# Kernel tuning notes

Measured on AMD Instinct MI355X. Metric: run time of the kernel, lower is better.

Reference implementation:

```python
import jax, jax.numpy as jnp
import numpy as np

LOG_STD_MAX = 2.0
LOG_STD_MIN = -5.0
N_EXPERTS = 16
TOPK = 4
OBS = 512
ACT = 256
BATCH = 16384


def setup_inputs() -> dict:
    key = jax.random.key(0)
    ks = jax.random.split(key, 7)
    s_obs = 1.0 / np.sqrt(OBS)
    return {
        "x": jax.random.normal(ks[0], (BATCH, OBS), dtype=jnp.float32),
        "router_w": jax.random.uniform(ks[1], (N_EXPERTS, OBS), jnp.float32, -s_obs, s_obs),
        "router_b": jax.random.uniform(ks[2], (N_EXPERTS,), jnp.float32, -s_obs, s_obs),
        "mean_w": jax.random.uniform(ks[3], (N_EXPERTS, ACT, OBS), jnp.float32, -s_obs, s_obs),
        "mean_b": jax.random.uniform(ks[4], (N_EXPERTS, ACT), jnp.float32, -s_obs, s_obs),
        "log_std_w": jax.random.uniform(ks[5], (N_EXPERTS, ACT, OBS), jnp.float32, -s_obs, s_obs),
        "log_std_b": jax.random.uniform(ks[6], (N_EXPERTS, ACT), jnp.float32, -s_obs, s_obs),
        "router_noise": 0,
    }


def reference(x, router_w, router_b, mean_w, mean_b, log_std_w, log_std_b, router_noise):
    # router_noise=0 -> deterministic path (training-time noise omitted)
    B = x.shape[0]
    router_logits = x @ router_w.T + router_b                    # [B, E]
    router_probs = jax.nn.softmax(router_logits, axis=-1)         # [B, E]
    topk_probs, topk_idx = jax.lax.top_k(router_probs, TOPK)      # [B, K]
    sparse_probs = jnp.zeros_like(router_probs).at[
        jnp.arange(B)[:, None], topk_idx
    ].set(topk_probs)                                             # [B, E]

    # all-expert dense stack: [B, E, A]
    expert_out = jnp.einsum("bo,eao->bea", x, mean_w) + mean_b
    log_std_out = jnp.einsum("bo,eao->bea", x, log_std_w) + log_std_b

    w = sparse_probs[:, :, None]                                  # [B, E, 1]
    mean = jnp.sum(expert_out * w, axis=1)                        # [B, A]
    log_std = jnp.sum(log_std_out * w, axis=1)                    # [B, A]
    log_std = jnp.tanh(log_std)
    log_std = LOG_STD_MIN + 0.5 * (LOG_STD_MAX - LOG_STD_MIN) * (log_std + 1.0)
    return mean, log_std
```

## Files before the change

### kernel.cpp

```cpp
#include <hip/hip_runtime.h>
#include <math.h>

#define BB   16384
#define OBS  512
#define NE   16
#define ACTD 256
#define TK   4

#define WS_ROWLIST_OFF  ((size_t)64)
#define WS_PROBLIST_OFF (WS_ROWLIST_OFF + (size_t)NE * BB * 4)
#define WS_SLOT_OFF     (WS_PROBLIST_OFF + (size_t)NE * BB * 4)
#define WS_XBF_OFF      (WS_SLOT_OFF + (size_t)NE * BB * 4)
#define WS_WM_OFF       (WS_XBF_OFF + (size_t)BB * OBS * 2)
#define WS_WL_OFF       (WS_WM_OFF + (size_t)NE * ACTD * OBS * 2)
#define WS_PART_OFF     (WS_WL_OFF + (size_t)NE * ACTD * OBS * 2)
#define WS_NEEDED_A2    (WS_PART_OFF + (size_t)2 * BB * TK * ACTD * 2)

typedef __attribute__((ext_vector_type(8))) short short8;
typedef __attribute__((ext_vector_type(4))) float floatx4;

__device__ __forceinline__ ushort f2bf(float f) {
    union { float f; unsigned u; } v; v.f = f;
    unsigned r = v.u + 0x7fffu + ((v.u >> 16) & 1u);
    return (ushort)(r >> 16);
}
__device__ __forceinline__ float bf2f(ushort u) {
    union { unsigned u; float f; } v; v.u = ((unsigned)u) << 16;
    return v.f;
}
__device__ __forceinline__ float lstd_act(float v) {
    return -5.f + 7.f * __builtin_amdgcn_rcpf(1.f + __expf(-2.f * v));
}

__global__ __launch_bounds__(256) void cvt2_bf16(
    const float* __restrict__ s0, const float* __restrict__ s1,
    ushort* __restrict__ d0, ushort* __restrict__ d1, int n4,
    int* __restrict__ counts)
{
    if (blockIdx.x == 0 && threadIdx.x < NE) counts[threadIdx.x] = 0;
    const int i = blockIdx.x * 256 + threadIdx.x;
    const float4* src = (i < n4) ? ((const float4*)s0 + i) : ((const float4*)s1 + (i - n4));
    ushort4* dst = (i < n4) ? ((ushort4*)d0 + i) : ((ushort4*)d1 + (i - n4));
    float4 v = *src;
    ushort4 o;
    o.x = f2bf(v.x); o.y = f2bf(v.y); o.z = f2bf(v.z); o.w = f2bf(v.w);
    *dst = o;
}

__global__ __launch_bounds__(256) void router_kernel(
    const float* __restrict__ x, const float* __restrict__ rw,
    const float* __restrict__ rb,
    int* __restrict__ counts, int* __restrict__ rowlist,
    float* __restrict__ problist, int* __restrict__ slot_of,
    ushort* __restrict__ xbf, int do_aux)
{
    __shared__ float wlds[NE * OBS];
    __shared__ int   lcnt[NE], lbase[NE];
    __shared__ int   s_e[64], s_lpos[64];
    __shared__ float s_p[64];

    const float4* rw4 = (const float4*)rw;
    float4* wl4 = (float4*)wlds;
    #pragma unroll
    for (int i = 0; i < 8; ++i) wl4[threadIdx.x + 256 * i] = rw4[threadIdx.x + 256 * i];
    if (threadIdx.x < NE) lcnt[threadIdx.x] = 0;
    __syncthreads();

    const int wave = threadIdx.x >> 6;
    const int lane = threadIdx.x & 63;
    const int q    = lane >> 4;
    const int i16  = lane & 15;
    const int row  = blockIdx.x * 16 + wave * 4 + q;

    const float4* xr = (const float4*)(x + (size_t)row * OBS);
    float4 xv[8];
    #pragma unroll
    for (int s = 0; s < 8; ++s) xv[s] = xr[s * 16 + i16];

    if (do_aux) {
        ushort4* xo = (ushort4*)(xbf + (size_t)row * OBS);
        #pragma unroll
        for (int s = 0; s < 8; ++s) {
            ushort4 o;
            o.x = f2bf(xv[s].x); o.y = f2bf(xv[s].y);
            o.z = f2bf(xv[s].z); o.w = f2bf(xv[s].w);
            xo[s * 16 + i16] = o;
        }
    }

    float p[NE];
    float m = -1e30f;
    #pragma unroll
    for (int e = 0; e < NE; ++e) {
        const float4* wep = (const float4*)(wlds + e * OBS);
        float d = 0.f;
        #pragma unroll
        for (int s = 0; s < 8; ++s) {
            float4 wv = wep[s * 16 + i16];
            d += xv[s].x * wv.x + xv[s].y * wv.y + xv[s].z * wv.z + xv[s].w * wv.w;
        }
        d += __shfl_xor(d, 1, 64);
        d += __shfl_xor(d, 2, 64);
        d += __shfl_xor(d, 4, 64);
        d += __shfl_xor(d, 8, 64);
        d += rb[e];
        p[e] = d;
        m = fmaxf(m, d);
    }
    float s = 0.f;
    #pragma unroll
    for (int e = 0; e < NE; ++e) { p[e] = __expf(p[e] - m); s += p[e]; }
    const float inv = 1.f / s;
    #pragma unroll
    for (int e = 0; e < NE; ++e) p[e] *= inv;

    int   sel_e[TK];
    float sel_p[TK];
    #pragma unroll
    for (int k = 0; k < TK; ++k) {
        float best = -1.f; int be = 0;
        #pragma unroll
        for (int e = 0; e < NE; ++e)
            if (p[e] > best) { best = p[e]; be = e; }
        sel_e[k] = be; sel_p[k] = best;
        #pragma unroll
        for (int e = 0; e < NE; ++e)
            if (e == be) p[e] = -2.f;
    }
    if (i16 < TK) {
        const int e = sel_e[i16];
        const int lpos = atomicAdd(&lcnt[e], 1);
        const int sid = (wave * 4 + q) * 4 + i16;
        s_e[sid] = e; s_p[sid] = sel_p[i16]; s_lpos[sid] = lpos;
    }
    __syncthreads();
    if (threadIdx.x < NE)
        lbase[threadIdx.x] = atomicAdd(&counts[threadIdx.x], lcnt[threadIdx.x]);
    __syncthreads();
    if (threadIdx.x < 64) {
        const int sid = threadIdx.x;
        const int e   = s_e[sid];
        const int pos = lbase[e] + s_lpos[sid];
        const int grow = blockIdx.x * 16 + (sid >> 2);
        rowlist[e * BB + pos]  = grow;
        problist[e * BB + pos] = s_p[sid];
        if (do_aux) slot_of[e * BB + pos] = grow * TK + (sid & 3);
    }
}

__global__ __launch_bounds__(256) void moe_gemm_64(
    const ushort* __restrict__ xbf,
    const ushort* __restrict__ wmean, const ushort* __restrict__ wlstd,
    const float* __restrict__ mean_b, const float* __restrict__ lstd_b,
    const int* __restrict__ counts, const int* __restrict__ rowlist,
    const float* __restrict__ problist, const int* __restrict__ slot_of,
    ushort* __restrict__ partial)
{
    const int e   = blockIdx.y;
    const int cnt = counts[e];
    const int tile0 = blockIdx.x * 64;
    if (tile0 >= cnt) return;

    const int zz    = blockIdx.z;
    const int which = zz >> 1;
    const int ctile = (zz & 1) * 128;
    const ushort* W   = (which ? wlstd : wmean) + (size_t)e * ACTD * OBS;
    const float* bias = (which ? lstd_b : mean_b) + e * ACTD + ctile;
    ushort* Pp = partial + (size_t)which * BB * TK * ACTD;

    __shared__ __align__(16) ushort xls[64 * 64];
    __shared__ __align__(16) ushort wls[128 * 64];
    __shared__ int   idx_l[64];
    __shared__ float probs_l[64];

    const int tid = threadIdx.x;
    const int l   = tid & 63;
    const int w   = tid >> 6;

    if (tid < 64) {
        const int pos = tile0 + tid;
        const bool v = pos < cnt;
        probs_l[tid] = v ? problist[e * BB + pos] : 0.f;
        idx_l[tid]   = v ? slot_of[e * BB + pos] : -1;
    }

    const int c_sw = (l & 7) ^ (l >> 3);
    const ushort* xp[2];
    #pragma unroll
    for (int i = 0; i < 2; ++i) {
        const int lrow = 16 * w + 8 * i + (l >> 3);
        const int pos  = tile0 + lrow;
        const int grow = (pos < cnt) ? rowlist[e * BB + pos] : rowlist[e * BB + tile0];
        xp[i] = xbf + (size_t)grow * OBS + c_sw * 8;
    }
    const ushort* wp[4];
    #pragma unroll
    for (int j = 0; j < 4; ++j) {
        const int col = ctile + 32 * w + 8 * j + (l >> 3);
        wp[j] = W + (size_t)col * OBS + c_sw * 8;
    }

    const int wm  = (w >> 1) * 32;
    const int wn  = (w & 1) * 64;
    const int rlo = l & 15;
    const int q   = l >> 4;
    const int r7  = rlo & 7;

    floatx4 acc[2][4];
    #pragma unroll
    for (int mi = 0; mi < 2; ++mi)
        #pragma unroll
        for (int ni = 0; ni < 4; ++ni)
            acc[mi][ni] = (floatx4){0.f, 0.f, 0.f, 0.f};

    for (int kt = 0; kt < OBS; kt += 64) {
        __syncthreads();
        #pragma unroll
        for (int i = 0; i < 2; ++i)
            __builtin_amdgcn_global_load_lds(
                (const __attribute__((address_space(1))) unsigned int*)(xp[i] + kt),
                (__attribute__((address_space(3))) unsigned int*)(xls + (2 * w + i) * 512),
                16, 0, 0);
        #pragma unroll
        for (int j = 0; j < 4; ++j)
            __builtin_amdgcn_global_load_lds(
                (const __attribute__((address_space(1))) unsigned int*)(wp[j] + kt),
                (__attribute__((address_space(3))) unsigned int*)(wls + (4 * w + j) * 512),
                16, 0, 0);
        __syncthreads();

        #pragma unroll
        for (int ks = 0; ks < 2; ++ks) {
            const int ch = (4 * ks + q) ^ r7;
            short8 af[2], bfr[4];
            #pragma unroll
            for (int mi = 0; mi < 2; ++mi)
                af[mi] = *(const short8*)(xls + (wm + mi * 16 + rlo) * 64 + ch * 8);
            #pragma unroll
            for (int ni = 0; ni < 4; ++ni)
                bfr[ni] = *(const short8*)(wls + (wn + ni * 16 + rlo) * 64 + ch * 8);
            #pragma unroll
            for (int mi = 0; mi < 2; ++mi)
                #pragma unroll
                for (int ni = 0; ni < 4; ++ni)
                    acc[mi][ni] = __builtin_amdgcn_mfma_f32_16x16x32_bf16(
                        af[mi], bfr[ni], acc[mi][ni], 0, 0, 0);
        }
    }

    #pragma unroll
    for (int mi = 0; mi < 2; ++mi) {
        #pragma unroll
        for (int r = 0; r < 4; ++r) {
            const int lrow = wm + mi * 16 + q * 4 + r;
            const int slot = idx_l[lrow];
            if (slot < 0) continue;
            const float pw = probs_l[lrow];
            ushort* orow = Pp + (size_t)slot * ACTD + ctile + wn + rlo;
            #pragma unroll
            for (int ni = 0; ni < 4; ++ni)
                orow[ni * 16] = f2bf(pw * (acc[mi][ni][r] + bias[wn + ni * 16 + rlo]));
        }
    }
}

__global__ __launch_bounds__(256) void combine_kernel(
    const ushort* __restrict__ partial, float* __restrict__ out)
{
    const int t  = blockIdx.x * 256 + threadIdx.x;
    const int r  = t >> 6;
    const int c4 = (t & 63) * 4;
    const ushort* Pm = partial;
    const ushort* Pl = partial + (size_t)BB * TK * ACTD;

    float m0 = 0.f, m1 = 0.f, m2 = 0.f, m3 = 0.f;
    float l0 = 0.f, l1 = 0.f, l2 = 0.f, l3 = 0.f;
    #pragma unroll
    for (int k = 0; k < TK; ++k) {
        const size_t off = (size_t)(r * TK + k) * ACTD + c4;
        ushort4 vm = *(const ushort4*)(Pm + off);
        ushort4 vl = *(const ushort4*)(Pl + off);
        m0 += bf2f(vm.x); m1 += bf2f(vm.y); m2 += bf2f(vm.z); m3 += bf2f(vm.w);
        l0 += bf2f(vl.x); l1 += bf2f(vl.y); l2 += bf2f(vl.z); l3 += bf2f(vl.w);
    }
    float4 mo = make_float4(m0, m1, m2, m3);
    float4 lo = make_float4(lstd_act(l0), lstd_act(l1), lstd_act(l2), lstd_act(l3));
    *(float4*)(out + (size_t)r * ACTD + c4) = mo;
    *(float4*)(out + (size_t)BB * ACTD + (size_t)r * ACTD + c4) = lo;
}

__global__ __launch_bounds__(256) void moe_gemm_f32(
    const float* __restrict__ x,
    const float* __restrict__ mean_w, const float* __restrict__ mean_b,
    const float* __restrict__ lstd_w, const float* __restrict__ lstd_b,
    const int* __restrict__ counts, const int* __restrict__ rowlist,
    const float* __restrict__ problist, float* __restrict__ out)
{
    const int e = blockIdx.y;
    const int cnt = counts[e];
    const int tile0 = blockIdx.x * 32;
    if (tile0 >= cnt) return;

    const int zz    = blockIdx.z;
    const int which = zz >> 1;
    const int ctile = (zz & 1) * 128;
    const float* W    = (which ? lstd_w : mean_w) + (size_t)e * ACTD * OBS;
    const float* bias = (which ? lstd_b : mean_b) + e * ACTD;
    float* outp = out + (size_t)which * BB * ACTD;

    __shared__ float xls[32][32];
    __shared__ float wls[32][128];

    const int sr  = threadIdx.x >> 3;
    const int skq = threadIdx.x & 7;
    int stage_row = -1;
    {
        const int pos = tile0 + sr;
        if (pos < cnt) stage_row = rowlist[e * BB + pos];
    }

    const int r0 = (threadIdx.x >> 5) << 2;
    const int c0 = (threadIdx.x & 31) << 2;

    float acc[4][4] = {};

    for (int kt = 0; kt < OBS; kt += 32) {
        __syncthreads();
        {
            float4 v = make_float4(0.f, 0.f, 0.f, 0.f);
            if (stage_row >= 0)
                v = *(const float4*)(x + (size_t)stage_row * OBS + kt + skq * 4);
            xls[skq * 4 + 0][sr] = v.x;
            xls[skq * 4 + 1][sr] = v.y;
            xls[skq * 4 + 2][sr] = v.z;
            xls[skq * 4 + 3][sr] = v.w;
        }
        #pragma unroll
        for (int j = 0; j < 4; ++j) {
            const int i  = threadIdx.x + 256 * j;
            const int c  = i >> 3;
            const int kq = i & 7;
            float4 v = *(const float4*)(W + (size_t)(ctile + c) * OBS + kt + kq * 4);
            wls[kq * 4 + 0][c] = v.x;
            wls[kq * 4 + 1][c] = v.y;
            wls[kq * 4 + 2][c] = v.z;
            wls[kq * 4 + 3][c] = v.w;
        }
        __syncthreads();

        #pragma unroll
        for (int k = 0; k < 32; ++k) {
            const float4 xa = *(const float4*)&xls[k][r0];
            const float4 wb = *(const float4*)&wls[k][c0];
            const float xv[4] = { xa.x, xa.y, xa.z, xa.w };
            const float wv[4] = { wb.x, wb.y, wb.z, wb.w };
            #pragma unroll
            for (int i = 0; i < 4; ++i)
                #pragma unroll
                for (int j = 0; j < 4; ++j)
                    acc[i][j] = fmaf(xv[i], wv[j], acc[i][j]);
        }
    }

    #pragma unroll
    for (int i = 0; i < 4; ++i) {
        const int pos = tile0 + r0 + i;
        if (pos >= cnt) break;
        const int grow = rowlist[e * BB + pos];
        const float pw = problist[e * BB + pos];
        float* orow = outp + (size_t)grow * ACTD + ctile + c0;
        #pragma unroll
        for (int j = 0; j < 4; ++j)
            atomicAdd(&orow[j], pw * (acc[i][j] + bias[ctile + c0 + j]));
    }
}

__global__ __launch_bounds__(256) void tanh_ep(float* __restrict__ out)
{
    const int i = blockIdx.x * 256 + threadIdx.x;
    float4* p = (float4*)(out + (size_t)BB * ACTD);
    float4 v = p[i];
    v.x = -5.f + 3.5f * (tanhf(v.x) + 1.f);
    v.y = -5.f + 3.5f * (tanhf(v.y) + 1.f);
    v.z = -5.f + 3.5f * (tanhf(v.z) + 1.f);
    v.w = -5.f + 3.5f * (tanhf(v.w) + 1.f);
    p[i] = v;
}

extern "C" void kernel_launch(void* const* d_in, const int* in_sizes, int n_in,
                              void* d_out, int out_size, void* d_ws, size_t ws_size,
                              hipStream_t stream)
{
    const float* x        = (const float*)d_in[0];
    const float* router_w = (const float*)d_in[1];
    const float* router_b = (const float*)d_in[2];
    const float* mean_w   = (const float*)d_in[3];
    const float* mean_b   = (const float*)d_in[4];
    const float* lstd_w   = (const float*)d_in[5];
    const float* lstd_b   = (const float*)d_in[6];

    float* out = (float*)d_out;
    int*    counts   = (int*)d_ws;
    int*    rowlist  = (int*)((char*)d_ws + WS_ROWLIST_OFF);
    float*  problist = (float*)((char*)d_ws + WS_PROBLIST_OFF);
    int*    slot_of  = (int*)((char*)d_ws + WS_SLOT_OFF);
    ushort* xbf      = (ushort*)((char*)d_ws + WS_XBF_OFF);
    ushort* wmbf     = (ushort*)((char*)d_ws + WS_WM_OFF);
    ushort* wlbf     = (ushort*)((char*)d_ws + WS_WL_OFF);
    ushort* partial  = (ushort*)((char*)d_ws + WS_PART_OFF);

    const bool tierA2 = (ws_size >= WS_NEEDED_A2);

    if (tierA2) {
        const int wn4 = NE * ACTD * OBS / 4;
        cvt2_bf16<<<2 * wn4 / 256, 256, 0, stream>>>(mean_w, lstd_w, wmbf, wlbf,
                                                     wn4, counts);

        router_kernel<<<BB / 16, 256, 0, stream>>>(x, router_w, router_b,
                                                   counts, rowlist, problist,
                                                   slot_of, xbf, 1);

        dim3 grid(BB / 64, NE, 4);
        moe_gemm_64<<<grid, 256, 0, stream>>>(xbf, wmbf, wlbf, mean_b, lstd_b,
                                              counts, rowlist, problist,
                                              slot_of, partial);
        combine_kernel<<<BB * 64 / 256, 256, 0, stream>>>(partial, out);
    } else {
        hipMemsetAsync(d_ws, 0, 64, stream);
        hipMemsetAsync(d_out, 0, (size_t)out_size * sizeof(float), stream);
        router_kernel<<<BB / 16, 256, 0, stream>>>(x, router_w, router_b,
                                                   counts, rowlist, problist,
                                                   (int*)nullptr, (ushort*)nullptr, 0);
        dim3 grid(BB / 32, NE, 4);
        moe_gemm_f32<<<grid, 256, 0, stream>>>(x, mean_w, mean_b, lstd_w, lstd_b,
                                               counts, rowlist, problist, out);
        tanh_ep<<<(BB * ACTD / 4) / 256, 256, 0, stream>>>(out);
    }
}
```

Baseline: 222.0 us.

## Fuse weight bf16 conversion into router and compact MoE GEMM grid

Moves the fp32-to-bf16 weight conversion into the router kernel's tail, so the separate conversion launch goes away and the counts reset becomes a memset. The expert GEMM grid shrinks from a dense per-expert grid, where many blocks exit early, to a compact 1040x4 grid. Each block finds its expert and tile by walking a prefix sum over the counts, and a swizzle spreads neighbouring blocks across experts and output tiles. The risks are extra per-block prefix-sum work and a fixed grid size that assumes at most 1040 row tiles in total.

```diff
diff --git a/kernel.cpp b/kernel.cpp
--- a/kernel.cpp
+++ b/kernel.cpp
@@ -32,27 +32,14 @@
     return -5.f + 7.f * __builtin_amdgcn_rcpf(1.f + __expf(-2.f * v));
 }
 
-__global__ __launch_bounds__(256) void cvt2_bf16(
-    const float* __restrict__ s0, const float* __restrict__ s1,
-    ushort* __restrict__ d0, ushort* __restrict__ d1, int n4,
-    int* __restrict__ counts)
-{
-    if (blockIdx.x == 0 && threadIdx.x < NE) counts[threadIdx.x] = 0;
-    const int i = blockIdx.x * 256 + threadIdx.x;
-    const float4* src = (i < n4) ? ((const float4*)s0 + i) : ((const float4*)s1 + (i - n4));
-    ushort4* dst = (i < n4) ? ((ushort4*)d0 + i) : ((ushort4*)d1 + (i - n4));
-    float4 v = *src;
-    ushort4 o;
-    o.x = f2bf(v.x); o.y = f2bf(v.y); o.z = f2bf(v.z); o.w = f2bf(v.w);
-    *dst = o;
-}
-
 __global__ __launch_bounds__(256) void router_kernel(
     const float* __restrict__ x, const float* __restrict__ rw,
     const float* __restrict__ rb,
     int* __restrict__ counts, int* __restrict__ rowlist,
     float* __restrict__ problist, int* __restrict__ slot_of,
-    ushort* __restrict__ xbf, int do_aux)
+    ushort* __restrict__ xbf,
+    const float* __restrict__ mwf, const float* __restrict__ lwf,
+    ushort* __restrict__ wmbf, ushort* __restrict__ wlbf, int do_aux)
 {
     __shared__ float wlds[NE * OBS];
     __shared__ int   lcnt[NE], lbase[NE];
@@ -146,6 +133,26 @@
         problist[e * BB + pos] = s_p[sid];
         if (do_aux) slot_of[e * BB + pos] = grow * TK + (sid & 3);
     }
+
+    if (do_aux) {
+        const int gid = blockIdx.x * 256 + threadIdx.x;
+        const float4* m4 = (const float4*)mwf;
+        const float4* l4 = (const float4*)lwf;
+        ushort4* mo = (ushort4*)wmbf;
+        ushort4* lo = (ushort4*)wlbf;
+        #pragma unroll
+        for (int j = 0; j < 2; ++j) {
+            const int idx = gid + 262144 * j;
+            float4 a = m4[idx];
+            ushort4 oa;
+            oa.x = f2bf(a.x); oa.y = f2bf(a.y); oa.z = f2bf(a.z); oa.w = f2bf(a.w);
+            mo[idx] = oa;
+            float4 b = l4[idx];
+            ushort4 ob;
+            ob.x = f2bf(b.x); ob.y = f2bf(b.y); ob.z = f2bf(b.z); ob.w = f2bf(b.w);
+            lo[idx] = ob;
+        }
+    }
 }
 
 __global__ __launch_bounds__(256) void moe_gemm_64(
@@ -156,12 +163,21 @@
     const float* __restrict__ problist, const int* __restrict__ slot_of,
     ushort* __restrict__ partial)
 {
-    const int e   = blockIdx.y;
-    const int cnt = counts[e];
-    const int tile0 = blockIdx.x * 64;
-    if (tile0 >= cnt) return;
-
-    const int zz    = blockIdx.z;
+    const int flat = blockIdx.x + 1040 * blockIdx.y;
+    const int virt = (flat & 7) * 520 + (flat >> 3);
+    const int zz   = virt & 3;
+    const int gt   = virt >> 2;
+
+    int e = -1, tile0 = 0, cnt = 0, tsum = 0;
+    #pragma unroll
+    for (int ee = 0; ee < NE; ++ee) {
+        const int ce = counts[ee];
+        const int nt = (ce + 63) >> 6;
+        if (e < 0 && gt < tsum + nt) { e = ee; tile0 = (gt - tsum) * 64; cnt = ce; }
+        tsum += nt;
+    }
+    if (e < 0) return;
+
     const int which = zz >> 1;
     const int ctile = (zz & 1) * 128;
     const ushort* W   = (which ? wlstd : wmean) + (size_t)e * ACTD * OBS;
@@ -412,15 +428,14 @@
     const bool tierA2 = (ws_size >= WS_NEEDED_A2);
 
     if (tierA2) {
-        const int wn4 = NE * ACTD * OBS / 4;
-        cvt2_bf16<<<2 * wn4 / 256, 256, 0, stream>>>(mean_w, lstd_w, wmbf, wlbf,
-                                                     wn4, counts);
+        hipMemsetAsync(d_ws, 0, 64, stream);
 
         router_kernel<<<BB / 16, 256, 0, stream>>>(x, router_w, router_b,
                                                    counts, rowlist, problist,
-                                                   slot_of, xbf, 1);
-
-        dim3 grid(BB / 64, NE, 4);
+                                                   slot_of, xbf,
+                                                   mean_w, lstd_w, wmbf, wlbf, 1);
+
+        dim3 grid(1040, 4);
         moe_gemm_64<<<grid, 256, 0, stream>>>(xbf, wmbf, wlbf, mean_b, lstd_b,
                                               counts, rowlist, problist,
                                               slot_of, partial);
@@ -430,7 +445,10 @@
         hipMemsetAsync(d_out, 0, (size_t)out_size * sizeof(float), stream);
         router_kernel<<<BB / 16, 256, 0, stream>>>(x, router_w, router_b,
                                                    counts, rowlist, problist,
-                                                   (int*)nullptr, (ushort*)nullptr, 0);
+                                                   (int*)nullptr, (ushort*)nullptr,
+                                                   (const float*)nullptr,
+                                                   (const float*)nullptr,
+                                                   (ushort*)nullptr, (ushort*)nullptr, 0);
         dim3 grid(BB / 32, NE, 4);
         moe_gemm_f32<<<grid, 256, 0, stream>>>(x, mean_w, mean_b, lstd_w, lstd_b,
                                                counts, rowlist, problist, out);
```

Result: faster. 196.7 us (-11.4%).
